# Kernel optimization log

Measured on AMD Instinct MI355X. Metric: run time of the kernel, lower is better.

Reference implementation:

```python
import jax, jax.numpy as jnp
import numpy as np

B, S, D = 4, 4096, 1024   # batch, seq_len, hidden_dim
E, K = 8, 2               # num_experts, num_experts_per_tok
H = 2 * D                 # expert MLP hidden dim


def setup_inputs() -> dict:
    key = jax.random.key(0)
    ks = jax.random.split(key, 4)
    sc = 0.02
    return {
        "hidden_states": jax.random.normal(ks[0], (B, S, D), jnp.float32),
        "Wr": (jax.random.normal(ks[1], (D, E), jnp.float32) * sc),
        "br": jnp.zeros((E,), jnp.float32),
        "W1": (jax.random.normal(ks[2], (E, D, H), jnp.float32) * sc),
        "b1": jnp.zeros((E, H), jnp.float32),
        "W2": (jax.random.normal(ks[3], (E, H, D), jnp.float32) * sc),
        "b2": jnp.zeros((E, D), jnp.float32),
    }


def reference(hidden_states, Wr, br, W1, b1, W2, b2):
    # Router: Linear -> Softmax (over experts), then top-k on the probabilities
    probs = jax.nn.softmax(hidden_states @ Wr + br, axis=-1)          # [B,S,E]
    top_w, top_i = jax.lax.top_k(probs, K)                            # [B,S,K]
    top_w = top_w / (top_w.sum(axis=-1, keepdims=True) + 1e-8)
    # Per-expert combine weight for every token (0 if expert not in top-k)
    combine = (jax.nn.one_hot(top_i, E, dtype=top_w.dtype)
               * top_w[..., None]).sum(axis=-2)                       # [B,S,E]
    # Reference semantics: run EVERY expert on EVERY token, then mask
    h = jnp.einsum('bsd,edh->ebsh', hidden_states, W1) + b1[:, None, None, :]  # [E,B,S,H]
    h = jax.nn.gelu(h, approximate=False)                             # exact GELU (torch default)
    expert_out = jnp.einsum('ebsh,ehd->ebsd', h, W2) + b2[:, None, None, :]    # [E,B,S,D]
    output = jnp.einsum('ebsd,bse->bsd', expert_out, combine)         # [B,S,D]
    return output
```

## Files before the change

kernel.cpp:

```cpp
#include <hip/hip_runtime.h>
#include <hip/hip_bf16.h>
#include <cstdint>
#include <cstddef>

#define TOKENS 16384
#define DIM    1024
#define NEXP   8
#define HID    2048
#define PAIRS  32768
#define PADCAP 33792
#define MTILES 264

typedef short     bf16x8 __attribute__((ext_vector_type(8)));
typedef float     f32x4  __attribute__((ext_vector_type(4)));

__device__ __forceinline__ unsigned short f2bf(float f) {
  union { float f; uint32_t u; } v; v.f = f;
  uint32_t u = v.u;
  uint32_t r = (u + 0x7FFFu + ((u >> 16) & 1u)) >> 16;
  return (unsigned short)r;
}

__device__ __forceinline__ void gload_lds16(const void* g, void* l) {
  __builtin_amdgcn_global_load_lds(
      (const __attribute__((address_space(1))) unsigned int*)g,
      (__attribute__((address_space(3))) unsigned int*)l,
      16, 0, 0);
}

__global__ __launch_bounds__(256) void tcvt(const float* __restrict__ src,
                                            unsigned short* __restrict__ dst,
                                            int R, int C) {
  __shared__ unsigned short t[64][72];
  const float* s = src + (size_t)blockIdx.z * R * C;
  unsigned short* d = dst + (size_t)blockIdx.z * R * C;
  int r0 = blockIdx.y * 64, c0 = blockIdx.x * 64;
  int tr = threadIdx.x >> 4;
  int tc = threadIdx.x & 15;
#pragma unroll
  for (int i = 0; i < 4; ++i) {
    int r = tr + i * 16;
    float4 v = *(const float4*)&s[(size_t)(r0 + r) * C + c0 + tc * 4];
    t[r][tc * 4 + 0] = f2bf(v.x);
    t[r][tc * 4 + 1] = f2bf(v.y);
    t[r][tc * 4 + 2] = f2bf(v.z);
    t[r][tc * 4 + 3] = f2bf(v.w);
  }
  __syncthreads();
#pragma unroll
  for (int i = 0; i < 4; ++i) {
    int c = tr + i * 16;
    ushort4 o;
    o.x = t[tc * 4 + 0][c];
    o.y = t[tc * 4 + 1][c];
    o.z = t[tc * 4 + 2][c];
    o.w = t[tc * 4 + 3][c];
    *(ushort4*)&d[(size_t)(c0 + c) * R + r0 + tc * 4] = o;
  }
}

__global__ __launch_bounds__(256) void router(const float* __restrict__ hs,
                                              const float* __restrict__ Wr,
                                              const float* __restrict__ br,
                                              unsigned short* __restrict__ Xb,
                                              int2* __restrict__ tok_e,
                                              float2* __restrict__ tok_w,
                                              int* __restrict__ counts) {
  __shared__ float wrT[NEXP][1032];
  __shared__ int hist[NEXP];
  int tid = threadIdx.x;
  if (tid < NEXP) hist[tid] = 0;
#pragma unroll
  for (int j = 0; j < 4; ++j) {
    int d = tid * 4 + j;
    float4 lo = *(const float4*)&Wr[d * 8];
    float4 hi = *(const float4*)&Wr[d * 8 + 4];
    wrT[0][d] = lo.x; wrT[1][d] = lo.y; wrT[2][d] = lo.z; wrT[3][d] = lo.w;
    wrT[4][d] = hi.x; wrT[5][d] = hi.y; wrT[6][d] = hi.z; wrT[7][d] = hi.w;
  }
  __syncthreads();
  int wave = tid >> 6, lane = tid & 63;

  for (int i = 0; i < 4; ++i) {
    int t = blockIdx.x * 16 + wave * 4 + i;
    float4 x[4];
#pragma unroll
    for (int p = 0; p < 4; ++p) {
      int d = p * 256 + lane * 4;
      x[p] = *(const float4*)&hs[(size_t)t * DIM + d];
      ushort4 o;
      o.x = f2bf(x[p].x); o.y = f2bf(x[p].y); o.z = f2bf(x[p].z); o.w = f2bf(x[p].w);
      *(ushort4*)&Xb[(size_t)t * DIM + d] = o;
    }
    float acc[NEXP];
#pragma unroll
    for (int e = 0; e < NEXP; ++e) {
      float a = 0.f;
#pragma unroll
      for (int p = 0; p < 4; ++p) {
        float4 w4 = *(const float4*)&wrT[e][p * 256 + lane * 4];
        a += x[p].x * w4.x + x[p].y * w4.y + x[p].z * w4.z + x[p].w * w4.w;
      }
      acc[e] = a;
    }
#pragma unroll
    for (int e = 0; e < NEXP; ++e) {
#pragma unroll
      for (int off = 32; off; off >>= 1) acc[e] += __shfl_xor(acc[e], off);
    }
    if (lane == 0) {
      float l[NEXP];
#pragma unroll
      for (int e = 0; e < NEXP; ++e) l[e] = acc[e] + br[e];
      float m = l[0];
#pragma unroll
      for (int e = 1; e < NEXP; ++e) m = fmaxf(m, l[e]);
      float p[NEXP], s = 0.f;
#pragma unroll
      for (int e = 0; e < NEXP; ++e) { p[e] = expf(l[e] - m); s += p[e]; }
      int e0 = 0;
#pragma unroll
      for (int e = 1; e < NEXP; ++e) if (p[e] > p[e0]) e0 = e;
      int e1 = (e0 == 0) ? 1 : 0;
#pragma unroll
      for (int e = 0; e < NEXP; ++e) if (e != e0 && p[e] > p[e1]) e1 = e;
      float q0 = p[e0] / s, q1 = p[e1] / s;
      float den = q0 + q1 + 1e-8f;
      tok_e[t] = make_int2(e0, e1);
      tok_w[t] = make_float2(q0 / den, q1 / den);
      atomicAdd(&hist[e0], 1);
      atomicAdd(&hist[e1], 1);
    }
  }
  __syncthreads();
  if (tid < NEXP)
    atomicAdd(&counts[(tid * 8 + (blockIdx.x & 7)) * 32], hist[tid]);
}

__global__ void mk_offsets(const int* __restrict__ counts, int* __restrict__ offs) {
  __shared__ int tot[NEXP];
  int e = threadIdx.x;
  if (e < NEXP) {
    int c = 0;
#pragma unroll
    for (int p = 0; p < 8; ++p) c += counts[(e * 8 + p) * 32];
    tot[e] = c;
  }
  __syncthreads();
  if (threadIdx.x == 0) {
    int o = 0;
#pragma unroll
    for (int i = 0; i < NEXP; ++i) {
      offs[i] = o;
      o += (tot[i] + 127) & ~127;
    }
    offs[NEXP] = o;
  }
}

__global__ __launch_bounds__(256) void scatter(const int2* __restrict__ tok_e,
                                               const float2* __restrict__ tok_w,
                                               const int* __restrict__ offs,
                                               int* __restrict__ gfill,
                                               int* __restrict__ ptok,
                                               float* __restrict__ pw) {
  __shared__ int lfill[NEXP], lbase[NEXP];
  int tid = threadIdx.x;
  if (tid < NEXP) lfill[tid] = 0;
  __syncthreads();
  int t = blockIdx.x * 256 + tid;
  int2 e = tok_e[t];
  float2 w = tok_w[t];
  int r0 = atomicAdd(&lfill[e.x], 1);
  int r1 = atomicAdd(&lfill[e.y], 1);
  __syncthreads();
  if (tid < NEXP) lbase[tid] = atomicAdd(&gfill[tid * 32], lfill[tid]);
  __syncthreads();
  int p0 = offs[e.x] + lbase[e.x] + r0;
  ptok[p0] = t; pw[p0] = w.x;
  int p1 = offs[e.y] + lbase[e.y] + r1;
  ptok[p1] = t; pw[p1] = w.y;
}

template <int MODE>
__global__ __launch_bounds__(256) void gemm_moe(
    const unsigned short* __restrict__ Asrc,
    const unsigned short* __restrict__ Bsrc,
    const float* __restrict__ bias,
    const int* __restrict__ offs,
    const int* __restrict__ ptok,
    const float* __restrict__ pw,
    unsigned short* __restrict__ Abuf,
    float* __restrict__ Out,
    int Ktot, int Ntot) {
  int row0 = blockIdx.y * 128;
  int padded_total = offs[NEXP];
  if (row0 >= padded_total) return;
  int e = 0;
  while (e < NEXP - 1 && row0 >= offs[e + 1]) ++e;
  int col0 = blockIdx.x * 128;

  __shared__ unsigned short As[2][128 * 64];
  __shared__ unsigned short Bs[2][128 * 64];
  __shared__ int   sTok[128];
  __shared__ float sW[128];

  int tid = threadIdx.x, wave = tid >> 6, lane = tid & 63;

  if (MODE == 1 && tid < 128) {
    sTok[tid] = ptok[row0 + tid];
    sW[tid]   = pw[row0 + tid];
  }

  int swz_src = (((lane & 7) ^ ((lane >> 3) & 7)) << 4);
  const char* aBase[4];
  const char* bBase[4];
#pragma unroll
  for (int i = 0; i < 4; ++i) {
    int r = wave * 32 + i * 8 + (lane >> 3);
    long arow;
    if (MODE == 0) arow = ptok[row0 + r];
    else           arow = row0 + r;
    aBase[i] = (const char*)Asrc + (size_t)arow * Ktot * 2 + swz_src;
    bBase[i] = (const char*)Bsrc + ((size_t)e * Ntot + col0 + r) * Ktot * 2 + swz_src;
  }

  f32x4 acc[4][4] = {};

  int wm = wave >> 1, wn = wave & 1;
  int rsel = lane & 15;
  int kblk = (lane >> 4) * 16;
  int rswz = (lane & 7) << 4;

#pragma unroll
  for (int i = 0; i < 4; ++i) {
    gload_lds16(aBase[i], &As[0][(wave * 32 + i * 8) * 64]);
    gload_lds16(bBase[i], &Bs[0][(wave * 32 + i * 8) * 64]);
  }
  __syncthreads();

  int cur = 0;
  for (int kt = 0; kt < Ktot; kt += 64, cur ^= 1) {
    if (kt + 64 < Ktot) {
      int nxt = cur ^ 1;
#pragma unroll
      for (int i = 0; i < 4; ++i) {
        gload_lds16(aBase[i] + (kt + 64) * 2, &As[nxt][(wave * 32 + i * 8) * 64]);
        gload_lds16(bBase[i] + (kt + 64) * 2, &Bs[nxt][(wave * 32 + i * 8) * 64]);
      }
    }
#pragma unroll
    for (int kk = 0; kk < 2; ++kk) {
      bf16x8 af[4], bfr[4];
#pragma unroll
      for (int i = 0; i < 4; ++i) {
        int row = wm * 64 + i * 16 + rsel;
        af[i] = *(const bf16x8*)((const char*)As[cur] + row * 128 + ((kk * 64 + kblk) ^ rswz));
      }
#pragma unroll
      for (int j = 0; j < 4; ++j) {
        int row = wn * 64 + j * 16 + rsel;
        bfr[j] = *(const bf16x8*)((const char*)Bs[cur] + row * 128 + ((kk * 64 + kblk) ^ rswz));
      }
#pragma unroll
      for (int i = 0; i < 4; ++i)
#pragma unroll
        for (int j = 0; j < 4; ++j)
          acc[i][j] = __builtin_amdgcn_mfma_f32_16x16x32_bf16(af[i], bfr[j], acc[i][j], 0, 0, 0);
    }
    __syncthreads();
  }

  int crow = (lane >> 4) * 4;
  int ccol = lane & 15;
#pragma unroll
  for (int i = 0; i < 4; ++i) {
#pragma unroll
    for (int j = 0; j < 4; ++j) {
      int gcol = col0 + wn * 64 + j * 16 + ccol;
      float bv = bias[(size_t)e * Ntot + gcol];
#pragma unroll
      for (int r = 0; r < 4; ++r) {
        int lrow = wm * 64 + i * 16 + crow + r;
        float v = acc[i][j][r] + bv;
        if (MODE == 0) {
          float g = 0.5f * v * (1.0f + erff(v * 0.70710678118654752f));
          Abuf[(size_t)(row0 + lrow) * HID + gcol] = f2bf(g);
        } else {
          atomicAdd(&Out[(size_t)sTok[lrow] * DIM + gcol], sW[lrow] * v);
        }
      }
    }
  }
}

extern "C" void kernel_launch(void* const* d_in, const int* in_sizes, int n_in,
                              void* d_out, int out_size, void* d_ws, size_t ws_size,
                              hipStream_t stream) {
  const float* hs = (const float*)d_in[0];
  const float* Wr = (const float*)d_in[1];
  const float* br = (const float*)d_in[2];
  const float* W1 = (const float*)d_in[3];
  const float* b1 = (const float*)d_in[4];
  const float* W2 = (const float*)d_in[5];
  const float* b2 = (const float*)d_in[6];
  float* out = (float*)d_out;

  char* ws = (char*)d_ws;
  unsigned short* W1bT = (unsigned short*)(ws);
  unsigned short* W2bT = (unsigned short*)(ws + 33554432);
  unsigned short* Xb   = (unsigned short*)(ws + 67108864);
  unsigned short* Abuf = (unsigned short*)(ws + 100663296);
  char* rb = ws + 239075328;
  int*    counts = (int*)(rb);
  int*    gfill  = (int*)(rb + 8192);
  int*    offs   = (int*)(rb + 9216);
  int2*   tok_e  = (int2*)(rb + 9344);
  float2* tok_w  = (float2*)(rb + 140416);
  int*    ptok   = (int*)(rb + 271488);
  float*  pw     = (float*)(rb + 406656);
  size_t routing_bytes = 541824;

  hipMemsetAsync(rb, 0, routing_bytes, stream);
  hipMemsetAsync(out, 0, (size_t)out_size * sizeof(float), stream);

  dim3 t1g(HID / 64, DIM / 64, NEXP);
  tcvt<<<t1g, 256, 0, stream>>>(W1, W1bT, DIM, HID);
  dim3 t2g(DIM / 64, HID / 64, NEXP);
  tcvt<<<t2g, 256, 0, stream>>>(W2, W2bT, HID, DIM);

  router<<<1024, 256, 0, stream>>>(hs, Wr, br, Xb, tok_e, tok_w, counts);
  mk_offsets<<<1, 64, 0, stream>>>(counts, offs);
  scatter<<<TOKENS / 256, 256, 0, stream>>>(tok_e, tok_w, offs, gfill, ptok, pw);

  dim3 g1(HID / 128, MTILES);
  gemm_moe<0><<<g1, 256, 0, stream>>>(Xb, W1bT, b1, offs, ptok, pw, Abuf, out, DIM, HID);
  dim3 g2(DIM / 128, MTILES);
  gemm_moe<1><<<g2, 256, 0, stream>>>(Abuf, W2bT, b2, offs, ptok, pw, Abuf, out, HID, DIM);
}
```

Measured before the change: 827.2 us.

## Enlarge MoE GEMM tiles to 256x256 with XCD-aware block remap and fast GELU

The grouped expert GEMMs move from 128x128 tiles with 256 threads to 256x256 tiles with 512 threads, and expert segments are padded to 256 rows. A flat grid is remapped so consecutive tiles land on the same XCD, which should improve L2 reuse. The exact erff GELU is replaced with a polynomial erf approximation using rcp and exp. The aim is more operand reuse per LDS load and a cheaper epilogue, at the cost of more padding waste, higher register pressure from 128 accumulator floats per thread, and roughly 1e-7 erf approximation error.

Result: faster. 775.7 us (-6.2%).

```diff
diff --git a/kernel.cpp b/kernel.cpp
--- a/kernel.cpp
+++ b/kernel.cpp
@@ -8,8 +8,8 @@
 #define NEXP   8
 #define HID    2048
 #define PAIRS  32768
-#define PADCAP 33792
-#define MTILES 264
+#define PADCAP 34816
+#define MT256  136
 
 typedef short     bf16x8 __attribute__((ext_vector_type(8)));
 typedef float     f32x4  __attribute__((ext_vector_type(4)));
@@ -19,6 +19,20 @@
   uint32_t u = v.u;
   uint32_t r = (u + 0x7FFFu + ((u >> 16) & 1u)) >> 16;
   return (unsigned short)r;
+}
+
+__device__ __forceinline__ float gelu_f(float v) {
+  float x = v * 0.70710678118654752f;
+  float ax = fabsf(x);
+  float t = __builtin_amdgcn_rcpf(1.0f + 0.3275911f * ax);
+  float p = t * (0.254829592f +
+           t * (-0.284496736f +
+           t * (1.421413741f +
+           t * (-1.453152027f +
+           t * 1.061405429f))));
+  float erfv = 1.0f - p * __expf(-ax * ax);
+  erfv = (x < 0.f) ? -erfv : erfv;
+  return 0.5f * v * (1.0f + erfv);
 }
 
 __device__ __forceinline__ void gload_lds16(const void* g, void* l) {
@@ -152,7 +166,7 @@
 #pragma unroll
     for (int i = 0; i < NEXP; ++i) {
       offs[i] = o;
-      o += (tot[i] + 127) & ~127;
+      o += (tot[i] + 255) & ~255;
     }
     offs[NEXP] = o;
   }
@@ -183,7 +197,7 @@
 }
 
 template <int MODE>
-__global__ __launch_bounds__(256) void gemm_moe(
+__global__ __launch_bounds__(512, 2) void gemm_moe(
     const unsigned short* __restrict__ Asrc,
     const unsigned short* __restrict__ Bsrc,
     const float* __restrict__ bias,
@@ -193,49 +207,53 @@
     unsigned short* __restrict__ Abuf,
     float* __restrict__ Out,
     int Ktot, int Ntot) {
-  int row0 = blockIdx.y * 128;
-  int padded_total = offs[NEXP];
-  if (row0 >= padded_total) return;
+  const int nx = Ntot >> 8;
+  int total = gridDim.x;
+  int bid = blockIdx.x;
+  int q = total >> 3, r8 = total & 7;
+  int xcd = bid & 7, idx = bid >> 3;
+  int wgid = (xcd < r8 ? xcd * (q + 1) : r8 * (q + 1) + (xcd - r8) * q) + idx;
+  int col0 = (wgid % nx) * 256;
+  int row0 = (wgid / nx) * 256;
+  if (row0 >= offs[NEXP]) return;
   int e = 0;
   while (e < NEXP - 1 && row0 >= offs[e + 1]) ++e;
-  int col0 = blockIdx.x * 128;
-
-  __shared__ unsigned short As[2][128 * 64];
-  __shared__ unsigned short Bs[2][128 * 64];
-  __shared__ int   sTok[128];
-  __shared__ float sW[128];
+
+  __shared__ unsigned short As[2][256 * 64];
+  __shared__ unsigned short Bs[2][256 * 64];
+  __shared__ int   sTok[256];
+  __shared__ float sW[256];
 
   int tid = threadIdx.x, wave = tid >> 6, lane = tid & 63;
 
-  if (MODE == 1 && tid < 128) {
+  if (MODE == 1 && tid < 256) {
     sTok[tid] = ptok[row0 + tid];
     sW[tid]   = pw[row0 + tid];
   }
 
   int swz_src = (((lane & 7) ^ ((lane >> 3) & 7)) << 4);
-  const char* aBase[4];
-  const char* bBase[4];
-#pragma unroll
-  for (int i = 0; i < 4; ++i) {
-    int r = wave * 32 + i * 8 + (lane >> 3);
-    long arow;
-    if (MODE == 0) arow = ptok[row0 + r];
-    else           arow = row0 + r;
-    aBase[i] = (const char*)Asrc + (size_t)arow * Ktot * 2 + swz_src;
-    bBase[i] = (const char*)Bsrc + ((size_t)e * Ntot + col0 + r) * Ktot * 2 + swz_src;
-  }
-
-  f32x4 acc[4][4] = {};
-
-  int wm = wave >> 1, wn = wave & 1;
+  size_t rowB = (size_t)Ktot * 2;
+  const char* aB[4];
+  const char* bB0 = (const char*)Bsrc +
+      ((size_t)e * Ntot + col0 + wave * 32 + (lane >> 3)) * rowB + swz_src;
+#pragma unroll
+  for (int i = 0; i < 4; ++i) {
+    int rr = wave * 32 + i * 8 + (lane >> 3);
+    long arow = (MODE == 0) ? (long)ptok[row0 + rr] : (long)(row0 + rr);
+    aB[i] = (const char*)Asrc + (size_t)arow * rowB + swz_src;
+  }
+
+  f32x4 acc[8][4] = {};
+
+  int wm = wave >> 2, wn = wave & 3;
   int rsel = lane & 15;
   int kblk = (lane >> 4) * 16;
   int rswz = (lane & 7) << 4;
 
 #pragma unroll
   for (int i = 0; i < 4; ++i) {
-    gload_lds16(aBase[i], &As[0][(wave * 32 + i * 8) * 64]);
-    gload_lds16(bBase[i], &Bs[0][(wave * 32 + i * 8) * 64]);
+    gload_lds16(aB[i], &As[0][(wave * 32 + i * 8) * 64]);
+    gload_lds16(bB0 + (size_t)i * 8 * rowB, &Bs[0][(wave * 32 + i * 8) * 64]);
   }
   __syncthreads();
 
@@ -245,16 +263,17 @@
       int nxt = cur ^ 1;
 #pragma unroll
       for (int i = 0; i < 4; ++i) {
-        gload_lds16(aBase[i] + (kt + 64) * 2, &As[nxt][(wave * 32 + i * 8) * 64]);
-        gload_lds16(bBase[i] + (kt + 64) * 2, &Bs[nxt][(wave * 32 + i * 8) * 64]);
+        gload_lds16(aB[i] + (kt + 64) * 2, &As[nxt][(wave * 32 + i * 8) * 64]);
+        gload_lds16(bB0 + (size_t)i * 8 * rowB + (kt + 64) * 2,
+                    &Bs[nxt][(wave * 32 + i * 8) * 64]);
       }
     }
 #pragma unroll
     for (int kk = 0; kk < 2; ++kk) {
-      bf16x8 af[4], bfr[4];
-#pragma unroll
-      for (int i = 0; i < 4; ++i) {
-        int row = wm * 64 + i * 16 + rsel;
+      bf16x8 af[8], bfr[4];
+#pragma unroll
+      for (int i = 0; i < 8; ++i) {
+        int row = wm * 128 + i * 16 + rsel;
         af[i] = *(const bf16x8*)((const char*)As[cur] + row * 128 + ((kk * 64 + kblk) ^ rswz));
       }
 #pragma unroll
@@ -263,7 +282,7 @@
         bfr[j] = *(const bf16x8*)((const char*)Bs[cur] + row * 128 + ((kk * 64 + kblk) ^ rswz));
       }
 #pragma unroll
-      for (int i = 0; i < 4; ++i)
+      for (int i = 0; i < 8; ++i)
 #pragma unroll
         for (int j = 0; j < 4; ++j)
           acc[i][j] = __builtin_amdgcn_mfma_f32_16x16x32_bf16(af[i], bfr[j], acc[i][j], 0, 0, 0);
@@ -274,18 +293,17 @@
   int crow = (lane >> 4) * 4;
   int ccol = lane & 15;
 #pragma unroll
-  for (int i = 0; i < 4; ++i) {
+  for (int i = 0; i < 8; ++i) {
 #pragma unroll
     for (int j = 0; j < 4; ++j) {
       int gcol = col0 + wn * 64 + j * 16 + ccol;
       float bv = bias[(size_t)e * Ntot + gcol];
 #pragma unroll
       for (int r = 0; r < 4; ++r) {
-        int lrow = wm * 64 + i * 16 + crow + r;
+        int lrow = wm * 128 + i * 16 + crow + r;
         float v = acc[i][j][r] + bv;
         if (MODE == 0) {
-          float g = 0.5f * v * (1.0f + erff(v * 0.70710678118654752f));
-          Abuf[(size_t)(row0 + lrow) * HID + gcol] = f2bf(g);
+          Abuf[(size_t)(row0 + lrow) * HID + gcol] = f2bf(gelu_f(v));
         } else {
           atomicAdd(&Out[(size_t)sTok[lrow] * DIM + gcol], sW[lrow] * v);
         }
@@ -311,15 +329,15 @@
   unsigned short* W2bT = (unsigned short*)(ws + 33554432);
   unsigned short* Xb   = (unsigned short*)(ws + 67108864);
   unsigned short* Abuf = (unsigned short*)(ws + 100663296);
-  char* rb = ws + 239075328;
+  char* rb = ws + 100663296 + (size_t)PADCAP * HID * 2;
   int*    counts = (int*)(rb);
   int*    gfill  = (int*)(rb + 8192);
   int*    offs   = (int*)(rb + 9216);
   int2*   tok_e  = (int2*)(rb + 9344);
   float2* tok_w  = (float2*)(rb + 140416);
   int*    ptok   = (int*)(rb + 271488);
-  float*  pw     = (float*)(rb + 406656);
-  size_t routing_bytes = 541824;
+  float*  pw     = (float*)(rb + 410752);
+  size_t routing_bytes = 550016;
 
   hipMemsetAsync(rb, 0, routing_bytes, stream);
   hipMemsetAsync(out, 0, (size_t)out_size * sizeof(float), stream);
@@ -333,8 +351,8 @@
   mk_offsets<<<1, 64, 0, stream>>>(counts, offs);
   scatter<<<TOKENS / 256, 256, 0, stream>>>(tok_e, tok_w, offs, gfill, ptok, pw);
 
-  dim3 g1(HID / 128, MTILES);
-  gemm_moe<0><<<g1, 256, 0, stream>>>(Xb, W1bT, b1, offs, ptok, pw, Abuf, out, DIM, HID);
-  dim3 g2(DIM / 128, MTILES);
-  gemm_moe<1><<<g2, 256, 0, stream>>>(Abuf, W2bT, b2, offs, ptok, pw, Abuf, out, HID, DIM);
-}
+  gemm_moe<0><<<(HID / 256) * MT256, 512, 0, stream>>>(Xb, W1bT, b1, offs, ptok, pw,
+                                                       Abuf, out, DIM, HID);
+  gemm_moe<1><<<(DIM / 256) * MT256, 512, 0, stream>>>(Abuf, W2bT, b2, offs, ptok, pw,
+                                                       Abuf, out, HID, DIM);
+}
```
